# Kernel optimization log

Hardware: AMD Instinct MI355X
Metric: run time of the kernel (lower is better)

## Reference

```python
import jax, jax.numpy as jnp
import numpy as np

# Module config (matches init_kwargs)
BATCH = 64
IN_CHANNELS, IN_H, IN_W = 64, 64, 64
OUT_CHANNELS = 256
KH, KW = 2, 2
SH, SW = 1, 1
DH, DW = 1, 1
# effective kernel size with dilation 1 is (2, 2); padding mode 'full' ->
# pad = (kaw-1, kaw-1, kah-1, kah-1) in torch F.pad order (left, right, top, bottom)
PAD_L, PAD_R, PAD_T, PAD_B = 1, 1, 1, 1
SEED = 42  # rand_state = np.random.RandomState(42)


def _make_weight():
    """Replicates the 0/1 selection-mask weight from SpatialProductLayer.__init__."""
    rs = np.random.RandomState(SEED)
    kernels_idx = []
    for _ in range(KH * KW):
        idx = np.arange(OUT_CHANNELS) % IN_CHANNELS
        rs.shuffle(idx)
        kernels_idx.append(idx)
    kernels_idx = np.stack(kernels_idx, axis=1)                       # (O, KH*KW)
    kernels_idx = kernels_idx.reshape(OUT_CHANNELS, 1, KH, KW)        # (O, 1, KH, KW)
    chan = np.arange(IN_CHANNELS).reshape(1, IN_CHANNELS, 1, 1)       # (1, I, 1, 1)
    weight = np.equal(chan, kernels_idx).astype(np.float32)           # (O, I, KH, KW), one-hot over I
    return jnp.asarray(weight)


def setup_inputs() -> dict:
    key = jax.random.key(0)
    x = jax.random.normal(key, (BATCH, IN_CHANNELS, IN_H, IN_W), dtype=jnp.float32)
    return {"x": x, "weight": _make_weight()}


def reference(x, weight):
    # x: (B, C, H, W). Pad exactly like torch.nn.functional.pad(x, (l, r, t, b)).
    xp = jnp.pad(x, ((0, 0), (0, 0), (PAD_T, PAD_B), (PAD_L, PAD_R)))
    # conv2d with stride/dilation; weight is the sparse 0/1 selection mask.
    out = jax.lax.conv_general_dilated(
        xp, weight,
        window_strides=(SH, SW),
        padding='VALID',
        rhs_dilation=(DH, DW),
        dimension_numbers=('NCHW', 'OIHW', 'NCHW'),
    )
    return out  # (B, 256, 65, 65)
```

## Files before the change

kernel.cpp:

```cpp
#include <hip/hip_runtime.h>

#define BATCH 64
#define IC    64
#define IH    64
#define IW    64
#define OC    256
#define OH    65
#define OW    65
#define NTAP  4
#define PLANE (OH * OW)

__global__ __launch_bounds__(256) void spl_kernel(
        const float* __restrict__ x,
        const float* __restrict__ w,
        float*       __restrict__ out) {
    const int o = blockIdx.x;
    const int b = blockIdx.y;
    const int t = threadIdx.x;

    __shared__ int idx_s[NTAP];
    float wv = w[o * (IC * NTAP) + t];
    if (wv > 0.5f) idx_s[t & 3] = t >> 2;
    __syncthreads();

    const size_t bbase = (size_t)b * IC * (IH * IW);
    const float* p00 = x + bbase + (size_t)idx_s[0] * (IH * IW);
    const float* p01 = x + bbase + (size_t)idx_s[1] * (IH * IW);
    const float* p10 = x + bbase + (size_t)idx_s[2] * (IH * IW);
    const float* p11 = x + bbase + (size_t)idx_s[3] * (IH * IW);
    float* po = out + ((size_t)b * OC + o) * PLANE;

    #pragma unroll 4
    for (int k = 0; k < 16; ++k) {
        int i = t + k * 256;
        int y  = (i * 4033) >> 18;
        int xx = i - y * 65;
        int off = (y << 6) + xx;
        bool yl = (y  >= 1), yh = (y  <= 63);
        bool xl = (xx >= 1), xh = (xx <= 63);
        float t00 = (yl && xl) ? p00[off - 65] : 0.0f;
        float t01 = (yl && xh) ? p01[off - 64] : 0.0f;
        float t10 = (yh && xl) ? p10[off - 1]  : 0.0f;
        float t11 = (yh && xh) ? p11[off]      : 0.0f;
        po[i] = (t00 + t01) + (t10 + t11);
    }
    {
        int i = t + 4096;
        if (i < PLANE) {
            int y  = (i * 4033) >> 18;
            int xx = i - y * 65;
            int off = (y << 6) + xx;
            bool yl = (y  >= 1), yh = (y  <= 63);
            bool xl = (xx >= 1), xh = (xx <= 63);
            float t00 = (yl && xl) ? p00[off - 65] : 0.0f;
            float t01 = (yl && xh) ? p01[off - 64] : 0.0f;
            float t10 = (yh && xl) ? p10[off - 1]  : 0.0f;
            float t11 = (yh && xh) ? p11[off]      : 0.0f;
            po[i] = (t00 + t01) + (t10 + t11);
        }
    }
}

extern "C" void kernel_launch(void* const* d_in, const int* in_sizes, int n_in,
                              void* d_out, int out_size, void* d_ws, size_t ws_size,
                              hipStream_t stream) {
    const float* x = (const float*)d_in[0];
    const float* w = (const float*)d_in[1];
    float* out     = (float*)d_out;

    dim3 grid(OC, BATCH);
    spl_kernel<<<grid, 256, 0, stream>>>(x, w, out);
}
```

Measured before the change: 426.7 us.

## Vectorize row-chunk loads/stores and remap blocks so each batch stays on one XCD

Each thread now handles a 4-wide chunk of an output row, using float4 unaligned loads of the four selected input channel rows and a float4 store, plus a scalar path for the last column. Border handling switches from per-load predication to clamped row indices and multiplicative masks. The grid becomes 1D and is remapped so the blocks for a given batch image run on the same XCD, which should improve L2 reuse of the input planes. The price is unaligned vector accesses and extra index arithmetic.

```diff
diff --git a/kernel.cpp b/kernel.cpp
--- a/kernel.cpp
+++ b/kernel.cpp
@@ -9,13 +9,25 @@
 #define OW    65
 #define NTAP  4
 #define PLANE (OH * OW)
+#define TASKS (OH * 17)
+
+__device__ __forceinline__ float4 ld4u(const float* p) {
+    float4 v; __builtin_memcpy(&v, p, 16); return v;
+}
+__device__ __forceinline__ void st4u(float* p, float4 v) {
+    __builtin_memcpy(p, &v, 16);
+}
 
 __global__ __launch_bounds__(256) void spl_kernel(
         const float* __restrict__ x,
         const float* __restrict__ w,
         float*       __restrict__ out) {
-    const int o = blockIdx.x;
-    const int b = blockIdx.y;
+    unsigned wg  = blockIdx.x;
+    unsigned xcd = wg & 7u;
+    unsigned l   = wg >> 3;
+    unsigned o   = l & 255u;
+    unsigned b   = ((l >> 8) << 3) | xcd;
+
     const int t = threadIdx.x;
 
     __shared__ int idx_s[NTAP];
@@ -30,33 +42,38 @@
     const float* p11 = x + bbase + (size_t)idx_s[3] * (IH * IW);
     float* po = out + ((size_t)b * OC + o) * PLANE;
 
-    #pragma unroll 4
-    for (int k = 0; k < 16; ++k) {
-        int i = t + k * 256;
-        int y  = (i * 4033) >> 18;
-        int xx = i - y * 65;
-        int off = (y << 6) + xx;
-        bool yl = (y  >= 1), yh = (y  <= 63);
-        bool xl = (xx >= 1), xh = (xx <= 63);
-        float t00 = (yl && xl) ? p00[off - 65] : 0.0f;
-        float t01 = (yl && xh) ? p01[off - 64] : 0.0f;
-        float t10 = (yh && xl) ? p10[off - 1]  : 0.0f;
-        float t11 = (yh && xh) ? p11[off]      : 0.0f;
-        po[i] = (t00 + t01) + (t10 + t11);
-    }
-    {
-        int i = t + 4096;
-        if (i < PLANE) {
-            int y  = (i * 4033) >> 18;
-            int xx = i - y * 65;
-            int off = (y << 6) + xx;
-            bool yl = (y  >= 1), yh = (y  <= 63);
-            bool xl = (xx >= 1), xh = (xx <= 63);
-            float t00 = (yl && xl) ? p00[off - 65] : 0.0f;
-            float t01 = (yl && xh) ? p01[off - 64] : 0.0f;
-            float t10 = (yh && xl) ? p10[off - 1]  : 0.0f;
-            float t11 = (yh && xh) ? p11[off]      : 0.0f;
-            po[i] = (t00 + t01) + (t10 + t11);
+    for (int base = 0; base < TASKS; base += 256) {
+        int i = base + t;
+        if (i >= TASKS) break;
+        int y = (i * 3856) >> 16;
+        int c = i - y * 17;
+
+        int   topr = (y >= 1)  ? (y - 1) : 0;
+        int   botr = (y <= 63) ? y       : 63;
+        float mt   = (y >= 1)  ? 1.0f : 0.0f;
+        float mb   = (y <= 63) ? 1.0f : 0.0f;
+        int to = topr << 6;
+        int bo = botr << 6;
+
+        if (c < 16) {
+            int x0  = c << 2;
+            int xm1 = (c == 0) ? 0 : (x0 - 1);
+            float4 tl = ld4u(p00 + to + xm1);
+            float4 tr = ld4u(p01 + to + x0);
+            float4 bl = ld4u(p10 + bo + xm1);
+            float4 br = ld4u(p11 + bo + x0);
+            if (c == 0) {
+                tl = make_float4(0.f, tl.x, tl.y, tl.z);
+                bl = make_float4(0.f, bl.x, bl.y, bl.z);
+            }
+            float4 r;
+            r.x = mt * (tl.x + tr.x) + mb * (bl.x + br.x);
+            r.y = mt * (tl.y + tr.y) + mb * (bl.y + br.y);
+            r.z = mt * (tl.z + tr.z) + mb * (bl.z + br.z);
+            r.w = mt * (tl.w + tr.w) + mb * (bl.w + br.w);
+            st4u(po + y * OW + x0, r);
+        } else {
+            po[y * OW + 64] = mt * p00[to + 63] + mb * p10[bo + 63];
         }
     }
 }
@@ -68,6 +85,5 @@
     const float* w = (const float*)d_in[1];
     float* out     = (float*)d_out;
 
-    dim3 grid(OC, BATCH);
-    spl_kernel<<<grid, 256, 0, stream>>>(x, w, out);
+    spl_kernel<<<OC * BATCH, 256, 0, stream>>>(x, w, out);
 }
```

Measured after the change: 409.5 us. 1.04x faster.
